# Optimization experiments

Hardware: AMD Instinct MI355X
Metric: run time of the kernel (lower is better)

## Reference

```python
import jax, jax.numpy as jnp
import numpy as np

SCALE = 65536          # Q16.16 fixed point, matching the torch module's SCALE
N_SEGMENTS = 16


def setup_inputs() -> dict:
    key = jax.random.key(0)
    k1, k2, k3, k4, k5 = jax.random.split(key, 5)
    # Large activation tensor -> memory-bound elementwise bucketize+affine.
    x = jax.random.normal(k1, (32, 4096, 1024), dtype=jnp.float32) * 2.0
    # n_segments-1 interior breakpoints, sorted, Q16.16 covering ~[-4, 4].
    breakpoints = jnp.sort(
        jax.random.randint(k2, (N_SEGMENTS - 1,), -4 * SCALE, 4 * SCALE, dtype=jnp.int32)
    )
    # Per-segment intercepts in Q16.16, within +/- 1.0 real units.
    intercepts = jax.random.randint(k3, (N_SEGMENTS,), -SCALE, SCALE, dtype=jnp.int32)
    # Per-segment slope signs in {-1, +1}.
    signs = 2 * jax.random.randint(k4, (N_SEGMENTS,), 0, 2, dtype=jnp.int32) - 1
    # Per-segment slope exponents: slope magnitude = 2^-exp (arithmetic right shift).
    exps = jax.random.randint(k5, (N_SEGMENTS,), 0, 8, dtype=jnp.int32)
    return {
        "x": x,
        "breakpoints": breakpoints,
        "intercepts": intercepts,
        "signs": signs,
        "exps": exps,
    }


def _plac_int32(x_q16, breakpoints, intercepts, signs, exps):
    # Bucketize each Q16.16 element against the sorted interior breakpoints;
    # seg in [0, n_segments-1].
    seg = jnp.searchsorted(breakpoints, x_q16, side="right").astype(jnp.int32)
    b = jnp.take(intercepts, seg)   # segment intercept (Q16.16)
    s = jnp.take(signs, seg)        # segment sign (+/-1)
    e = jnp.take(exps, seg)         # segment slope exponent
    # y = intercept + sign * (x >> exp) in int32 Q16.16 (arithmetic shift).
    return b + s * jnp.right_shift(x_q16, e)


def reference(x, breakpoints, intercepts, signs, exps):
    # Faithful to torch forward: detach, quantize to Q16.16 int32, eval, dequantize.
    x_q16 = (jax.lax.stop_gradient(x).astype(jnp.float32) * SCALE).astype(jnp.int32)
    y_q16 = _plac_int32(x_q16, breakpoints, intercepts, signs, exps)
    return (y_q16.astype(jnp.float32) / SCALE).astype(x.dtype)
```

## Files before the change

### kernel.cpp

```cpp
#include <hip/hip_runtime.h>

#define NSEG 16

typedef float f32x4 __attribute__((ext_vector_type(4)));

__device__ __forceinline__ float plac_one(float xv, const float* __restrict__ bpf,
                                          const f32x4* __restrict__ s_tab) {
    float t = truncf(xv * 65536.0f);
    int seg = 0;
    #pragma unroll
    for (int k = 0; k < 15; ++k) seg += (t >= bpf[k]);
    f32x4 c = s_tab[seg];
    float u = floorf(t * c.z);
    return fmaf(c.y, u, c.x);
}

__global__ __launch_bounds__(256) void plac_kernel(
    const float* __restrict__ x,
    const int* __restrict__ bps,
    const int* __restrict__ intercepts,
    const int* __restrict__ signs,
    const int* __restrict__ exps,
    float* __restrict__ out,
    long long n4,
    long long n)
{
    __shared__ f32x4 s_tab[NSEG];

    const int tid = threadIdx.x;
    if (tid < NSEG) {
        float b  = (float)intercepts[tid] * (1.0f / 65536.0f);
        float s  = (float)signs[tid]      * (1.0f / 65536.0f);
        float ei = __int_as_float((127 - exps[tid]) << 23);
        f32x4 row = {b, s, ei, 0.0f};
        s_tab[tid] = row;
    }
    __syncthreads();

    float bpf[15];
    #pragma unroll
    for (int k = 0; k < 15; ++k) bpf[k] = (float)bps[k];

    const f32x4* __restrict__ x4 = (const f32x4*)x;
    f32x4* __restrict__ o4 = (f32x4*)out;

    long long nchunks = n4 >> 10;
    for (long long cидx = blockIdx.x; cидx < nchunks; cидx += gridDim.x) {
        long long base = (cидx << 10) + tid;
        f32x4 v0 = x4[base];
        f32x4 v1 = x4[base + 256];
        f32x4 v2 = x4[base + 512];
        f32x4 v3 = x4[base + 768];
        f32x4 r0, r1, r2, r3;
        #pragma unroll
        for (int j = 0; j < 4; ++j) r0[j] = plac_one(v0[j], bpf, s_tab);
        #pragma unroll
        for (int j = 0; j < 4; ++j) r1[j] = plac_one(v1[j], bpf, s_tab);
        #pragma unroll
        for (int j = 0; j < 4; ++j) r2[j] = plac_one(v2[j], bpf, s_tab);
        #pragma unroll
        for (int j = 0; j < 4; ++j) r3[j] = plac_one(v3[j], bpf, s_tab);
        o4[base]       = r0;
        o4[base + 256] = r1;
        o4[base + 512] = r2;
        o4[base + 768] = r3;
    }

    long long start = nchunks << 10;
    for (long long i = start + (long long)blockIdx.x * blockDim.x + tid;
         i < n4; i += (long long)gridDim.x * blockDim.x) {
        f32x4 v = x4[i];
        f32x4 r;
        #pragma unroll
        for (int j = 0; j < 4; ++j) r[j] = plac_one(v[j], bpf, s_tab);
        o4[i] = r;
    }

    if (blockIdx.x == 0) {
        long long base = n4 * 4;
        for (long long ii = base + tid; ii < n; ii += blockDim.x) {
            out[ii] = plac_one(x[ii], bpf, s_tab);
        }
    }
}

extern "C" void kernel_launch(void* const* d_in, const int* in_sizes, int n_in,
                              void* d_out, int out_size, void* d_ws, size_t ws_size,
                              hipStream_t stream) {
    const float* x          = (const float*)d_in[0];
    const int*   bps        = (const int*)d_in[1];
    const int*   intercepts = (const int*)d_in[2];
    const int*   signs      = (const int*)d_in[3];
    const int*   exps       = (const int*)d_in[4];
    float* out = (float*)d_out;

    long long n  = (long long)out_size;
    long long n4 = n / 4;

    const int block = 256;
    int grid = 2048;
    long long nchunks = n4 >> 10;
    if (nchunks < grid) {
        long long blocks_needed = (n4 + block - 1) / block;
        if (blocks_needed < 1) blocks_needed = 1;
        if (blocks_needed < grid) grid = (int)blocks_needed;
    }

    plac_kernel<<<grid, block, 0, stream>>>(x, bps, intercepts, signs, exps,
                                            out, n4, n);
}
```

Before: 219.8 us.

## Replace linear breakpoint scan with shared-memory bucket LUT lookup

Builds a per-block shared-memory lookup table indexed by a power-of-two bucket of the quantized input, sized so that each bucket holds at most one breakpoint. Each element then needs one LUT read and one compare instead of fifteen compares. If the breakpoint gaps are too small for the table size, it falls back to the full scan. The change also drops the 4-way unrolled chunk loop in favour of a plain grid-stride loop and adds an occupancy hint to launch bounds. In exchange, every block pays a LUT-building cost, and the kernel gains an extra dependent shared-memory load per element on what is a memory-bound operation.

New measurement: 211.1 us. 1.04x faster.

```diff
diff --git a/kernel.cpp b/kernel.cpp
--- a/kernel.cpp
+++ b/kernel.cpp
@@ -1,33 +1,74 @@
 #include <hip/hip_runtime.h>
+#include <limits.h>
+#include <math.h>
 
 #define NSEG 16
+#define LMAX 2048
 
 typedef float f32x4 __attribute__((ext_vector_type(4)));
+typedef float f32x2 __attribute__((ext_vector_type(2)));
 
-__device__ __forceinline__ float plac_one(float xv, const float* __restrict__ bpf,
-                                          const f32x4* __restrict__ s_tab) {
+__device__ __forceinline__ float plac_tail(float t, f32x4 c) {
+    float u = floorf(t * c.z);
+    return fmaf(c.y, u, c.x);
+}
+
+__device__ __forceinline__ float plac_lut_one(float xv, const f32x2* __restrict__ s_lut,
+                                              const f32x4* __restrict__ s_tab,
+                                              int LOm, int S, int Lm1) {
+    float t = truncf(xv * 65536.0f);
+    int xq = (int)t;
+    int idx = (xq - LOm) >> S;
+    idx = min(max(idx, 0), Lm1);
+    f32x2 e = s_lut[idx];
+    int m = __float_as_int(e.y);
+    int seg = m + (t >= e.x ? 1 : 0);
+    return plac_tail(t, s_tab[seg]);
+}
+
+__device__ __forceinline__ float plac_full_one(float xv, const float* __restrict__ bpf,
+                                               const f32x4* __restrict__ s_tab) {
     float t = truncf(xv * 65536.0f);
     int seg = 0;
     #pragma unroll
     for (int k = 0; k < 15; ++k) seg += (t >= bpf[k]);
-    f32x4 c = s_tab[seg];
-    float u = floorf(t * c.z);
-    return fmaf(c.y, u, c.x);
+    return plac_tail(t, s_tab[seg]);
 }
 
-__global__ __launch_bounds__(256) void plac_kernel(
+__global__ __launch_bounds__(256, 8) void plac_kernel(
     const float* __restrict__ x,
     const int* __restrict__ bps,
     const int* __restrict__ intercepts,
     const int* __restrict__ signs,
     const int* __restrict__ exps,
     float* __restrict__ out,
-    long long n4,
-    long long n)
+    long long n4, long long n)
 {
+    __shared__ f32x2 s_lut[LMAX];
     __shared__ f32x4 s_tab[NSEG];
 
     const int tid = threadIdx.x;
+
+    int bp[15];
+    #pragma unroll
+    for (int k = 0; k < 15; ++k) bp[k] = bps[k];
+    int gapmin = INT_MAX;
+    #pragma unroll
+    for (int k = 0; k < 14; ++k) gapmin = min(gapmin, bp[k + 1] - bp[k]);
+    const int LO = bp[0];
+    const int range = bp[14] - bp[0];
+    int Smin = 0;
+    while (((range >> Smin) + 2) > LMAX) ++Smin;
+    int S = 0;
+    bool valid = false;
+    if (gapmin > 0) {
+        S = 31 - __clz(gapmin);
+        valid = (S >= Smin);
+    }
+    const int L   = (range >> S) + 2;
+    const int Lm1 = L - 1;
+    const int LOm = LO - (1 << S);
+
     if (tid < NSEG) {
         float b  = (float)intercepts[tid] * (1.0f / 65536.0f);
         float s  = (float)signs[tid]      * (1.0f / 65536.0f);
@@ -35,51 +76,60 @@
         f32x4 row = {b, s, ei, 0.0f};
         s_tab[tid] = row;
     }
+
+    if (valid) {
+        for (int i = tid; i < L; i += 256) {
+            int m = 0;
+            float bpn = INFINITY;
+            if (i > 0) {
+                int left = LO + ((i - 1) << S);
+                #pragma unroll
+                for (int k = 14; k >= 0; --k) {
+                    if (bp[k] <= left) m += 1;
+                    else               bpn = (float)bp[k];
+                }
+            } else {
+                bpn = (float)bp[0];
+            }
+            f32x2 e = {bpn, __int_as_float(m)};
+            s_lut[i] = e;
+        }
+    }
     __syncthreads();
-
-    float bpf[15];
-    #pragma unroll
-    for (int k = 0; k < 15; ++k) bpf[k] = (float)bps[k];
 
     const f32x4* __restrict__ x4 = (const f32x4*)x;
     f32x4* __restrict__ o4 = (f32x4*)out;
+    long long i0     = (long long)blockIdx.x * blockDim.x + tid;
+    long long stride = (long long)gridDim.x * blockDim.x;
 
-    long long nchunks = n4 >> 10;
-    for (long long cидx = blockIdx.x; cидx < nchunks; cидx += gridDim.x) {
-        long long base = (cидx << 10) + tid;
-        f32x4 v0 = x4[base];
-        f32x4 v1 = x4[base + 256];
-        f32x4 v2 = x4[base + 512];
-        f32x4 v3 = x4[base + 768];
-        f32x4 r0, r1, r2, r3;
+    if (valid) {
+        for (long long i = i0; i < n4; i += stride) {
+            f32x4 v = x4[i];
+            f32x4 r;
+            #pragma unroll
+            for (int j = 0; j < 4; ++j)
+                r[j] = plac_lut_one(v[j], s_lut, s_tab, LOm, S, Lm1);
+            o4[i] = r;
+        }
+        if (blockIdx.x == 0) {
+            for (long long ii = n4 * 4 + tid; ii < n; ii += blockDim.x)
+                out[ii] = plac_lut_one(x[ii], s_lut, s_tab, LOm, S, Lm1);
+        }
+    } else {
+        float bpf[15];
         #pragma unroll
-        for (int j = 0; j < 4; ++j) r0[j] = plac_one(v0[j], bpf, s_tab);
-        #pragma unroll
-        for (int j = 0; j < 4; ++j) r1[j] = plac_one(v1[j], bpf, s_tab);
-        #pragma unroll
-        for (int j = 0; j < 4; ++j) r2[j] = plac_one(v2[j], bpf, s_tab);
-        #pragma unroll
-        for (int j = 0; j < 4; ++j) r3[j] = plac_one(v3[j], bpf, s_tab);
-        o4[base]       = r0;
-        o4[base + 256] = r1;
-        o4[base + 512] = r2;
-        o4[base + 768] = r3;
-    }
-
-    long long start = nchunks << 10;
-    for (long long i = start + (long long)blockIdx.x * blockDim.x + tid;
-         i < n4; i += (long long)gridDim.x * blockDim.x) {
-        f32x4 v = x4[i];
-        f32x4 r;
-        #pragma unroll
-        for (int j = 0; j < 4; ++j) r[j] = plac_one(v[j], bpf, s_tab);
-        o4[i] = r;
-    }
-
-    if (blockIdx.x == 0) {
-        long long base = n4 * 4;
-        for (long long ii = base + tid; ii < n; ii += blockDim.x) {
-            out[ii] = plac_one(x[ii], bpf, s_tab);
+        for (int k = 0; k < 15; ++k) bpf[k] = (float)bp[k];
+        for (long long i = i0; i < n4; i += stride) {
+            f32x4 v = x4[i];
+            f32x4 r;
+            #pragma unroll
+            for (int j = 0; j < 4; ++j)
+                r[j] = plac_full_one(v[j], bpf, s_tab);
+            o4[i] = r;
+        }
+        if (blockIdx.x == 0) {
+            for (long long ii = n4 * 4 + tid; ii < n; ii += blockDim.x)
+                out[ii] = plac_full_one(x[ii], bpf, s_tab);
         }
     }
 }
@@ -98,13 +148,9 @@
     long long n4 = n / 4;
 
     const int block = 256;
-    int grid = 2048;
-    long long nchunks = n4 >> 10;
-    if (nchunks < grid) {
-        long long blocks_needed = (n4 + block - 1) / block;
-        if (blocks_needed < 1) blocks_needed = 1;
-        if (blocks_needed < grid) grid = (int)blocks_needed;
-    }
+    long long blocks_needed = (n4 + block - 1) / block;
+    if (blocks_needed < 1) blocks_needed = 1;
+    int grid = (int)((blocks_needed < 2048) ? blocks_needed : 2048);
 
     plac_kernel<<<grid, block, 0, stream>>>(x, bps, intercepts, signs, exps,
                                             out, n4, n);
```
